# Kernel optimization log

Hardware: AMD Instinct MI355X
Metric: run time of the kernel (lower is better)

## Reference

```python
import jax, jax.numpy as jnp
import numpy as np

FIXED_DELTA_LAMBDA = 0.04226162119141463


def setup_inputs() -> dict:
    key = jax.random.key(0)
    B, H, W, S = 4, 512, 512, 128
    L_hr = jax.random.normal(key, (B, H, W, S), dtype=jnp.float32)
    # HyPlant FLUO-like spectral grid: 670-780 nm
    sensor_wavelengths = jnp.linspace(670.0, 780.0, S, dtype=jnp.float32)
    return {
        "L_hr": L_hr,
        "delta_lambda": jnp.float32(0.0),
        "delta_sigma": jnp.float32(0.0),
        "sensor_wavelengths": sensor_wavelengths,
    }


def reference(L_hr, delta_lambda, delta_sigma, sensor_wavelengths):
    # L_hr: [B, H, W, spec]; output: [B, spec, H, W]
    n = sensor_wavelengths.shape[0]
    wl_min = sensor_wavelengths.min()
    wl_max = sensor_wavelengths.max()
    high_res = (wl_max - wl_min) / n  # matches (max-min)/len in __init__
    # lambda_hr = linspace(wl_min, wl_max, n) with traced endpoints
    lambda_hr = wl_min + (wl_max - wl_min) * jnp.arange(n, dtype=L_hr.dtype) / (n - 1)

    sigma = (0.27 + delta_sigma) * 2.3548
    # NOTE: the torch module also computes a Gaussian conv1d blur (L_blur) that is
    # never used in the output (dead code); we faithfully reproduce the output math.
    # delta_lambda is also unused: the module applies fixed_delta_lambda instead.
    effective_wl = sensor_wavelengths + FIXED_DELTA_LAMBDA  # [spec]
    diff = lambda_hr[None, :] - effective_wl[:, None]       # [spec, spec]
    g = jnp.exp(-0.5 * (diff / sigma) ** 2)
    g = g / (g.sum(axis=1, keepdims=True) + 1e-6)
    # 'ij,bjhw->bihw' after permute(0,3,1,2) == 'ij,bhwj->bihw' on the raw layout
    return jnp.einsum("ij,bhwj->bihw", g, L_hr) * high_res
```

## Files before the change

kernel.cpp:

```cpp
#include <hip/hip_runtime.h>
#include <hip/hip_bf16.h>


#define S_CH   128
#define HW_PLN (512 * 512)
#define TPX    64
#define RS     137
#define NTAP   9
#define RADIUS 4

__global__ void hyplant_taps_kernel(const float* __restrict__ sw,
                                    const float* __restrict__ dsig,
                                    float* __restrict__ w_out) {
    const int i = threadIdx.x;
    const int n = S_CH;
    float wl_min = sw[0], wl_max = sw[0];
    for (int j = 1; j < n; ++j) {
        float v = sw[j];
        wl_min = fminf(wl_min, v);
        wl_max = fmaxf(wl_max, v);
    }
    const float span     = wl_max - wl_min;
    const float high_res = span / (float)n;
    const float sigma    = (0.27f + dsig[0]) * 2.3548f;
    const float inv_s    = 1.0f / sigma;
    const float ewl      = sw[i] + 0.04226162119141463f;

    float sum = 0.0f;
    for (int j = 0; j < n; ++j) {
        float lhr = wl_min + (span * (float)j) / 127.0f;
        float d   = (lhr - ewl) * inv_s;
        sum += expf(-0.5f * d * d);
    }
    const float scale = high_res / (sum + 1e-6f);

    for (int t = 0; t < NTAP; ++t) {
        int   j = i - RADIUS + t;
        float w = 0.0f;
        if (j >= 0 && j < n) {
            float lhr = wl_min + (span * (float)j) / 127.0f;
            float d   = (lhr - ewl) * inv_s;
            w = expf(-0.5f * d * d) * scale;
        }
        w_out[i * NTAP + t] = w;
    }
}

__global__ __launch_bounds__(256) void hyplant_sim_kernel(
        const float* __restrict__ L,
        const float* __restrict__ w_g,
        float* __restrict__ out) {
    __shared__ float lds[TPX * RS];

    const int bid = blockIdx.x;
    const int b   = bid >> 12;
    const int hw0 = (bid & 4095) << 6;
    const int tid = threadIdx.x;

    for (int idx = tid; idx < TPX * 8; idx += 256) {
        int row = idx >> 3, q = idx & 7;
        lds[row * RS + (q < 4 ? q : 128 + q)] = 0.0f;
    }

    const float4* src = (const float4*)(L + ((size_t)b * HW_PLN + hw0) * S_CH);
    for (int idx = tid; idx < TPX * 32; idx += 256) {
        int    p  = idx >> 5, f4 = idx & 31;
        float4 v  = src[p * 32 + f4];
        int    ba = p * RS + RADIUS + f4 * 4;
        lds[ba]     = v.x;
        lds[ba + 1] = v.y;
        lds[ba + 2] = v.z;
        lds[ba + 3] = v.w;
    }
    __syncthreads();

    const int p = tid & 63;
    const int c = __builtin_amdgcn_readfirstlane((tid >> 6) << 5);

    float r[32 + 2 * RADIUS];
    const int rb = p * RS + c;
#pragma unroll
    for (int k = 0; k < 32 + 2 * RADIUS; ++k) r[k] = lds[rb + k];

    const float* __restrict__ wg = w_g + c * NTAP;

    float* outp = out + ((size_t)(b * S_CH + c)) * HW_PLN + hw0 + p;
#pragma unroll
    for (int il = 0; il < 32; ++il) {
        float acc = 0.0f;
#pragma unroll
        for (int t = 0; t < NTAP; ++t)
            acc = fmaf(wg[il * NTAP + t], r[il + t], acc);
        __builtin_nontemporal_store(acc, outp + (size_t)il * HW_PLN);
    }
}

extern "C" void kernel_launch(void* const* d_in, const int* in_sizes, int n_in,
                              void* d_out, int out_size, void* d_ws, size_t ws_size,
                              hipStream_t stream) {
    const float* L    = (const float*)d_in[0];
    const float* dsig = (const float*)d_in[2];
    const float* sw   = (const float*)d_in[3];
    float*       out  = (float*)d_out;
    float*       taps = (float*)d_ws;

    hyplant_taps_kernel<<<1, 128, 0, stream>>>(sw, dsig, taps);

    const int total_pixels = in_sizes[0] / S_CH;
    const int grid         = total_pixels / TPX;
    hyplant_sim_kernel<<<grid, 256, 0, stream>>>(L, taps, out);
}
```

Measured before the change: 214.2 us.

## Tile by channel slices over 512-pixel blocks with transposed LDS staging

Each block now handles 512 pixels for a 16-channel output slice, loading a 24-channel haloed window per pixel into a channel-major shared array instead of staging full 128-channel spectra for 64 pixels. Each thread computes two adjacent pixels and writes them as 8-byte nontemporal stores, which widens the output write transactions. The cost is extra input traffic, because halo channels are reloaded by neighbouring slices (24 loaded per 16 produced). The input reads also become partial 96-byte segments per pixel, which may coalesce less well.

```diff
diff --git a/kernel.cpp b/kernel.cpp
--- a/kernel.cpp
+++ b/kernel.cpp
@@ -4,10 +4,14 @@
 
 #define S_CH   128
 #define HW_PLN (512 * 512)
-#define TPX    64
-#define RS     137
 #define NTAP   9
 #define RADIUS 4
+#define PXB    512
+#define SLICE  24
+#define CST    514
+#define CW     16
+
+typedef float v2f __attribute__((ext_vector_type(2)));
 
 __global__ void hyplant_taps_kernel(const float* __restrict__ sw,
                                     const float* __restrict__ dsig,
@@ -50,48 +54,59 @@
         const float* __restrict__ L,
         const float* __restrict__ w_g,
         float* __restrict__ out) {
-    __shared__ float lds[TPX * RS];
+    __shared__ float sm[SLICE * CST];
 
     const int bid = blockIdx.x;
-    const int b   = bid >> 12;
-    const int hw0 = (bid & 4095) << 6;
+    const int s   = bid & 7;
+    const int rr  = bid >> 3;
+    const int b   = rr >> 9;
+    const int hw0 = (rr & 511) << 9;
     const int tid = threadIdx.x;
+    const int c   = s << 4;
+    const int cb  = c - RADIUS;
 
-    for (int idx = tid; idx < TPX * 8; idx += 256) {
-        int row = idx >> 3, q = idx & 7;
-        lds[row * RS + (q < 4 ? q : 128 + q)] = 0.0f;
-    }
-
-    const float4* src = (const float4*)(L + ((size_t)b * HW_PLN + hw0) * S_CH);
-    for (int idx = tid; idx < TPX * 32; idx += 256) {
-        int    p  = idx >> 5, f4 = idx & 31;
-        float4 v  = src[p * 32 + f4];
-        int    ba = p * RS + RADIUS + f4 * 4;
-        lds[ba]     = v.x;
-        lds[ba + 1] = v.y;
-        lds[ba + 2] = v.z;
-        lds[ba + 3] = v.w;
+    const float* base = L + ((size_t)b * HW_PLN + hw0) * S_CH;
+#pragma unroll
+    for (int k = 0; k < 12; ++k) {
+        int idx  = tid + (k << 8);
+        int px   = idx / 6;
+        int ch   = (idx - px * 6) << 2;
+        int jsrc = cb + ch;
+        float4 v = make_float4(0.f, 0.f, 0.f, 0.f);
+        if (jsrc >= 0 && jsrc <= S_CH - 4)
+            v = *(const float4*)(base + (size_t)px * S_CH + jsrc);
+        sm[(ch    ) * CST + px] = v.x;
+        sm[(ch + 1) * CST + px] = v.y;
+        sm[(ch + 2) * CST + px] = v.z;
+        sm[(ch + 3) * CST + px] = v.w;
     }
     __syncthreads();
 
-    const int p = tid & 63;
-    const int c = __builtin_amdgcn_readfirstlane((tid >> 6) << 5);
+    const int w  = tid >> 6;
+    const int l  = tid & 63;
+    const int p0 = (w << 7) + (l << 1);
 
-    float r[32 + 2 * RADIUS];
-    const int rb = p * RS + c;
+    float r0[SLICE], r1[SLICE];
 #pragma unroll
-    for (int k = 0; k < 32 + 2 * RADIUS; ++k) r[k] = lds[rb + k];
+    for (int k = 0; k < SLICE; ++k) {
+        r0[k] = sm[k * CST + p0];
+        r1[k] = sm[k * CST + p0 + 1];
+    }
 
     const float* __restrict__ wg = w_g + c * NTAP;
 
-    float* outp = out + ((size_t)(b * S_CH + c)) * HW_PLN + hw0 + p;
+    float* outp = out + ((size_t)(b * S_CH + c)) * HW_PLN + hw0 + p0;
 #pragma unroll
-    for (int il = 0; il < 32; ++il) {
-        float acc = 0.0f;
+    for (int il = 0; il < CW; ++il) {
+        float a0 = 0.0f, a1 = 0.0f;
 #pragma unroll
-        for (int t = 0; t < NTAP; ++t)
-            acc = fmaf(wg[il * NTAP + t], r[il + t], acc);
-        __builtin_nontemporal_store(acc, outp + (size_t)il * HW_PLN);
+        for (int t = 0; t < NTAP; ++t) {
+            float wt = wg[il * NTAP + t];
+            a0 = fmaf(wt, r0[il + t], a0);
+            a1 = fmaf(wt, r1[il + t], a1);
+        }
+        v2f o; o.x = a0; o.y = a1;
+        __builtin_nontemporal_store(o, (v2f*)(outp + (size_t)il * HW_PLN));
     }
 }
 
@@ -107,6 +122,6 @@
     hyplant_taps_kernel<<<1, 128, 0, stream>>>(sw, dsig, taps);
 
     const int total_pixels = in_sizes[0] / S_CH;
-    const int grid         = total_pixels / TPX;
+    const int grid         = (total_pixels / PXB) * 8;
     hyplant_sim_kernel<<<grid, 256, 0, stream>>>(L, taps, out);
 }
```

Measured after the change: 359.6 us. 1.68x slower.
